# Kernel optimization log

Measured on AMD Instinct MI355X. Metric: run time of the kernel, lower is better.

The kernel has to match this reference:

```python
import jax, jax.numpy as jnp
jax.config.update("jax_enable_x64", True)
import numpy as np

B, IN_DIM, OUT_DIM = 65536, 256, 256
SCALE = 100.0


def setup_inputs() -> dict:
    key = jax.random.key(0)
    k1, k2, k3 = jax.random.split(key, 3)
    c_x = jax.random.randint(k1, (B, IN_DIM), 0, 200, dtype=jnp.int64)
    weight = jax.random.normal(k2, (OUT_DIM, IN_DIM), dtype=jnp.float32)
    true_bias = jax.random.normal(k3, (OUT_DIM,), dtype=jnp.float32)
    in_scale = jnp.ones((1,), dtype=jnp.float32) * jnp.float32(SCALE)
    return {"c_x": c_x, "weight": weight, "true_bias": true_bias, "in_scale": in_scale}


def scale_round(x, scale):
    # torch.round(x * scale).long()
    return jnp.round(x * scale).astype(jnp.int64)


def reference(c_x, weight, true_bias, in_scale):
    scale = jnp.float32(SCALE)
    s = in_scale[0]
    # quantize weight (done in __init__ in the original) and bias (done per-forward)
    w_q = scale_round(weight, scale)                 # [OUT, IN] int64
    b_q = scale_round(true_bias, s * scale)          # [OUT] int64
    # fhe.matrix_product(W, x.T).T == x @ W.T, then add_matrix_vector adds bias per row
    out = jnp.matmul(c_x, w_q.T) + b_q[None, :]      # [B, OUT] int64
    return out, s * scale
```

## Files before the change

kernel.cpp:

```cpp
#include <hip/hip_runtime.h>

typedef _Float16 half8 __attribute__((ext_vector_type(8)));
typedef float floatx4 __attribute__((ext_vector_type(4)));

#define IN_DIM 256
#define OUT_DIM 256
#define M_TILE 32

__global__ void quant_kernel(const float* __restrict__ w,
                             const float* __restrict__ bias,
                             const float* __restrict__ in_scale,
                             _Float16* __restrict__ wqp,
                             float* __restrict__ bq,
                             float* __restrict__ out_scalar) {
    int t = blockIdx.x * blockDim.x + threadIdx.x;
    if (t < (OUT_DIM * IN_DIM) / 8) {
        int lane = t & 63;
        int ks   = (t >> 6) & 7;
        int ct   = t >> 9;
        int row  = ct * 16 + (lane & 15);
        int k0   = ks * 32 + (lane >> 4) * 8;
        const float* src = w + row * IN_DIM + k0;
        half8 h;
#pragma unroll
        for (int e = 0; e < 8; ++e)
            h[e] = (_Float16)rintf(src[e] * 100.0f);
        *((half8*)wqp + t) = h;
    }
    if (t < OUT_DIM) {
        float s2 = in_scale[0] * 100.0f;
        bq[t] = rintf(bias[t] * s2);
    }
    if (t == 0 && out_scalar != nullptr)
        out_scalar[0] = in_scale[0] * 100.0f;
}

__device__ __forceinline__ void gl_lds16(const int* g, int* lds_row_base) {
    __builtin_amdgcn_global_load_lds(
        (const __attribute__((address_space(1))) void*)g,
        (__attribute__((address_space(3))) void*)lds_row_base,
        16, 0, 0);
}

__global__ __launch_bounds__(256, 4) void gemm_kernel(const int* __restrict__ cx,
                                                      const _Float16* __restrict__ wqp,
                                                      const float* __restrict__ bq,
                                                      float* __restrict__ out) {
    __shared__ int ctile[M_TILE * IN_DIM];

    const int t    = threadIdx.x;
    const int wave = t >> 6;
    const int lane = t & 63;
    const int m16  = lane & 15;
    const int quad = lane >> 4;

    const size_t m0 = (size_t)blockIdx.x * M_TILE;

    {
        const int* gbase = cx + (m0 + wave * 8) * IN_DIM;
#pragma unroll
        for (int i = 0; i < 8; ++i) {
            const int* g = gbase + i * IN_DIM + ((lane ^ i) << 2);
            gl_lds16(g, &ctile[(wave * 8 + i) * IN_DIM]);
        }
    }

    const half8* wbase = (const half8*)wqp;
    half8 acur[4], anext[4];
#pragma unroll
    for (int i = 0; i < 4; ++i)
        acur[i] = wbase[((wave * 4 + i) * 8 + 0) * 64 + lane];

    __syncthreads();

    floatx4 acc[4][2] = {};
    const int s = m16 & 7;

#pragma unroll
    for (int ks = 0; ks < 8; ++ks) {
        if (ks < 7) {
#pragma unroll
            for (int i = 0; i < 4; ++i)
                anext[i] = wbase[((wave * 4 + i) * 8 + (ks + 1)) * 64 + lane];
        }

        const int pos0 = ((ks * 8 + quad * 2) ^ s) << 2;
        const int pos1 = pos0 ^ 4;
        half8 bfr[2];
#pragma unroll
        for (int j = 0; j < 2; ++j) {
            const int rb = (j * 16 + m16) * IN_DIM;
            int4 lo = *(const int4*)&ctile[rb + pos0];
            int4 hi = *(const int4*)&ctile[rb + pos1];
            half8 b;
            b[0] = (_Float16)lo.x; b[1] = (_Float16)lo.y;
            b[2] = (_Float16)lo.z; b[3] = (_Float16)lo.w;
            b[4] = (_Float16)hi.x; b[5] = (_Float16)hi.y;
            b[6] = (_Float16)hi.z; b[7] = (_Float16)hi.w;
            bfr[j] = b;
        }

#pragma unroll
        for (int i = 0; i < 4; ++i)
#pragma unroll
            for (int j = 0; j < 2; ++j)
                acc[i][j] = __builtin_amdgcn_mfma_f32_16x16x32_f16(acur[i], bfr[j], acc[i][j], 0, 0, 0);

#pragma unroll
        for (int i = 0; i < 4; ++i) acur[i] = anext[i];
    }

#pragma unroll
    for (int i = 0; i < 4; ++i) {
        int col = wave * 64 + i * 16 + quad * 4;
        floatx4 bv = *(const floatx4*)(bq + col);
#pragma unroll
        for (int j = 0; j < 2; ++j) {
            size_t row = m0 + j * 16 + m16;
            *(floatx4*)(out + row * OUT_DIM + col) = acc[i][j] + bv;
        }
    }
}

extern "C" void kernel_launch(void* const* d_in, const int* in_sizes, int n_in,
                              void* d_out, int out_size, void* d_ws, size_t ws_size,
                              hipStream_t stream) {
    const int*   cx       = (const int*)d_in[0];
    const float* w        = (const float*)d_in[1];
    const float* bias     = (const float*)d_in[2];
    const float* in_scale = (const float*)d_in[3];
    float* out = (float*)d_out;

    _Float16* wqp = (_Float16*)d_ws;
    float*    bq  = (float*)((char*)d_ws + OUT_DIM * IN_DIM * 2);

    const int rows = in_sizes[0] / IN_DIM;
    const size_t gemm_elems = (size_t)rows * OUT_DIM;
    float* out_scalar = ((size_t)out_size > gemm_elems) ? (out + gemm_elems) : nullptr;

    quant_kernel<<<32, 256, 0, stream>>>(w, bias, in_scale, wqp, bq, out_scalar);
    gemm_kernel<<<rows / M_TILE, 256, 0, stream>>>(cx, wqp, bq, out);
}
```

Baseline: 132.5 us.

## Double-buffer two 32-row tiles per block, overlapping second load with first compute

```diff
diff --git a/kernel.cpp b/kernel.cpp
--- a/kernel.cpp
+++ b/kernel.cpp
@@ -5,7 +5,7 @@
 
 #define IN_DIM 256
 #define OUT_DIM 256
-#define M_TILE 32
+#define ROWSTR_I 264
 
 __global__ void quant_kernel(const float* __restrict__ w,
                              const float* __restrict__ bias,
@@ -42,11 +42,62 @@
         16, 0, 0);
 }
 
-__global__ __launch_bounds__(256, 4) void gemm_kernel(const int* __restrict__ cx,
+__device__ __forceinline__ half8 cvt_frag(const int* __restrict__ rowp, int kb) {
+    int4 lo = *(const int4*)(rowp + kb);
+    int4 hi = *(const int4*)(rowp + kb + 4);
+    half8 b;
+    b[0] = (_Float16)lo.x; b[1] = (_Float16)lo.y;
+    b[2] = (_Float16)lo.z; b[3] = (_Float16)lo.w;
+    b[4] = (_Float16)hi.x; b[5] = (_Float16)hi.y;
+    b[6] = (_Float16)hi.z; b[7] = (_Float16)hi.w;
+    return b;
+}
+
+__device__ __forceinline__ void pass_compute(const int* __restrict__ buf,
+                                             const half8* __restrict__ wbase,
+                                             int wave, int lane, int m16, int quad,
+                                             floatx4 (&acc)[4][2]) {
+#pragma unroll
+    for (int ks = 0; ks < 8; ++ks) {
+        half8 afr[4];
+#pragma unroll
+        for (int i = 0; i < 4; ++i)
+            afr[i] = wbase[((wave * 4 + i) * 8 + ks) * 64 + lane];
+        const int kb = ks * 32 + quad * 8;
+        half8 bfr[2];
+#pragma unroll
+        for (int j = 0; j < 2; ++j)
+            bfr[j] = cvt_frag(buf + (j * 16 + m16) * ROWSTR_I, kb);
+#pragma unroll
+        for (int i = 0; i < 4; ++i)
+#pragma unroll
+            for (int j = 0; j < 2; ++j)
+                acc[i][j] = __builtin_amdgcn_mfma_f32_16x16x32_f16(afr[i], bfr[j], acc[i][j], 0, 0, 0);
+    }
+}
+
+__device__ __forceinline__ void pass_store(float* __restrict__ out, size_t row0,
+                                           const float* __restrict__ bq,
+                                           int wave, int m16, int quad,
+                                           floatx4 (&acc)[4][2]) {
+#pragma unroll
+    for (int i = 0; i < 4; ++i) {
+        int col = wave * 64 + i * 16 + quad * 4;
+        floatx4 bv = *(const floatx4*)(bq + col);
+#pragma unroll
+        for (int j = 0; j < 2; ++j) {
+            size_t row = row0 + j * 16 + m16;
+            *(floatx4*)(out + row * OUT_DIM + col) = acc[i][j] + bv;
+        }
+    }
+}
+
+__global__ __launch_bounds__(256, 2) void gemm_kernel(const int* __restrict__ cx,
                                                       const _Float16* __restrict__ wqp,
                                                       const float* __restrict__ bq,
                                                       float* __restrict__ out) {
-    __shared__ int ctile[M_TILE * IN_DIM];
+    __shared__ int bufA[32 * ROWSTR_I];
+    __shared__ int bufB[32 * ROWSTR_I];
 
     const int t    = threadIdx.x;
     const int wave = t >> 6;
@@ -54,72 +105,34 @@
     const int m16  = lane & 15;
     const int quad = lane >> 4;
 
-    const size_t m0 = (size_t)blockIdx.x * M_TILE;
+    const size_t m0 = (size_t)blockIdx.x * 64;
+    const half8* wbase = (const half8*)wqp;
 
     {
-        const int* gbase = cx + (m0 + wave * 8) * IN_DIM;
+        const int* g = cx + (m0 + wave * 8) * IN_DIM + lane * 4;
 #pragma unroll
-        for (int i = 0; i < 8; ++i) {
-            const int* g = gbase + i * IN_DIM + ((lane ^ i) << 2);
-            gl_lds16(g, &ctile[(wave * 8 + i) * IN_DIM]);
-        }
+        for (int i = 0; i < 8; ++i)
+            gl_lds16(g + i * IN_DIM, &bufA[(wave * 8 + i) * ROWSTR_I]);
+    }
+    __syncthreads();
+
+    {
+        const int* g = cx + (m0 + 32 + wave * 8) * IN_DIM + lane * 4;
+#pragma unroll
+        for (int i = 0; i < 8; ++i)
+            gl_lds16(g + i * IN_DIM, &bufB[(wave * 8 + i) * ROWSTR_I]);
     }
 
-    const half8* wbase = (const half8*)wqp;
-    half8 acur[4], anext[4];
-#pragma unroll
-    for (int i = 0; i < 4; ++i)
-        acur[i] = wbase[((wave * 4 + i) * 8 + 0) * 64 + lane];
+    floatx4 accA[4][2] = {};
+    pass_compute(bufA, wbase, wave, lane, m16, quad, accA);
 
     __syncthreads();
 
-    floatx4 acc[4][2] = {};
-    const int s = m16 & 7;
+    pass_store(out, m0, bq, wave, m16, quad, accA);
 
-#pragma unroll
-    for (int ks = 0; ks < 8; ++ks) {
-        if (ks < 7) {
-#pragma unroll
-            for (int i = 0; i < 4; ++i)
-                anext[i] = wbase[((wave * 4 + i) * 8 + (ks + 1)) * 64 + lane];
-        }
-
-        const int pos0 = ((ks * 8 + quad * 2) ^ s) << 2;
-        const int pos1 = pos0 ^ 4;
-        half8 bfr[2];
-#pragma unroll
-        for (int j = 0; j < 2; ++j) {
-            const int rb = (j * 16 + m16) * IN_DIM;
-            int4 lo = *(const int4*)&ctile[rb + pos0];
-            int4 hi = *(const int4*)&ctile[rb + pos1];
-            half8 b;
-            b[0] = (_Float16)lo.x; b[1] = (_Float16)lo.y;
-            b[2] = (_Float16)lo.z; b[3] = (_Float16)lo.w;
-            b[4] = (_Float16)hi.x; b[5] = (_Float16)hi.y;
-            b[6] = (_Float16)hi.z; b[7] = (_Float16)hi.w;
-            bfr[j] = b;
-        }
-
-#pragma unroll
-        for (int i = 0; i < 4; ++i)
-#pragma unroll
-            for (int j = 0; j < 2; ++j)
-                acc[i][j] = __builtin_amdgcn_mfma_f32_16x16x32_f16(acur[i], bfr[j], acc[i][j], 0, 0, 0);
-
-#pragma unroll
-        for (int i = 0; i < 4; ++i) acur[i] = anext[i];
-    }
-
-#pragma unroll
-    for (int i = 0; i < 4; ++i) {
-        int col = wave * 64 + i * 16 + quad * 4;
-        floatx4 bv = *(const floatx4*)(bq + col);
-#pragma unroll
-        for (int j = 0; j < 2; ++j) {
-            size_t row = m0 + j * 16 + m16;
-            *(floatx4*)(out + row * OUT_DIM + col) = acc[i][j] + bv;
-        }
-    }
+    floatx4 accB[4][2] = {};
+    pass_compute(bufB, wbase, wave, lane, m16, quad, accB);
+    pass_store(out, m0 + 32, bq, wave, m16, quad, accB);
 }
 
 extern "C" void kernel_launch(void* const* d_in, const int* in_sizes, int n_in,
@@ -139,5 +152,5 @@
     float* out_scalar = ((size_t)out_size > gemm_elems) ? (out + gemm_elems) : nullptr;
 
     quant_kernel<<<32, 256, 0, stream>>>(w, bias, in_scale, wqp, bq, out_scalar);
-    gemm_kernel<<<rows / M_TILE, 256, 0, stream>>>(cx, wqp, bq, out);
+    gemm_kernel<<<rows / 64, 256, 0, stream>>>(cx, wqp, bq, out);
 }
```

Result: slower. 139.0 us (+4.9%).
